# Kernel optimization log

Hardware: AMD Instinct MI355X
Metric: run time of the kernel (lower is better)

Reference implementation:

```python
import jax, jax.numpy as jnp
import numpy as np

RBF_DIM = 64          # args.radius_emb_dim
FOLD_DIM = 128        # args.fold_dim
PROT_RADIUS = 30.0    # args.protein_radius (GaussianSmearing stop)
NP_, NL_, E_ = 100000, 50000, 500000


def gaussian_smearing(d):
    # GaussianSmearing(start=0, stop=PROT_RADIUS, num_gaussians=RBF_DIM)
    offsets = jnp.linspace(0.0, PROT_RADIUS, RBF_DIM, dtype=d.dtype)  # [R]
    coeff = -0.5 / (offsets[1] - offsets[0]) ** 2
    return jnp.exp(coeff * (d[:, None] - offsets[None, :]) ** 2)  # [E, R]


def setup_inputs() -> dict:
    key = jax.random.key(0)
    ks = jax.random.split(key, 12)
    scale = 10.0  # spread positions so distances span [0, PROT_RADIUS]
    pos = lambda k, n: jax.random.normal(k, (n, 3), jnp.float32) * scale
    inp = {
        'lig_pos': pos(ks[0], NL_),
        'prot_pos': pos(ks[1], NP_),
        'prot_pos_Cb': pos(ks[2], NP_),
        'prot_pos_C': pos(ks[3], NP_),
        'prot_pos_O': pos(ks[4], NP_),
        'prot_pos_N': pos(ks[5], NP_),
        'W1': jax.random.normal(ks[6], (5 * RBF_DIM, FOLD_DIM), jnp.float32) * 0.05,
        'b1': jnp.zeros((FOLD_DIM,), jnp.float32),
        'W2': jax.random.normal(ks[7], (FOLD_DIM, FOLD_DIM), jnp.float32) * 0.05,
        'b2': jnp.zeros((FOLD_DIM,), jnp.float32),
        'src': jax.random.randint(ks[8], (E_,), 0, NL_, jnp.int32),   # ligand index per edge
        'dst': jax.random.randint(ks[9], (E_,), 0, NP_, jnp.int32),   # protein index per edge
    }
    return inp


def reference(lig_pos, prot_pos, prot_pos_Cb, prot_pos_C, prot_pos_O, prot_pos_N,
              W1, b1, W2, b2, src, dst):
    lp = lig_pos[src]  # [E, 3] gather of ligand positions
    # 5 distance channels: CA/Cb/C/O/N protein atoms, each RBF-smeared
    feats = [gaussian_smearing(jnp.linalg.norm(lp - p[dst], axis=-1))
             for p in (prot_pos, prot_pos_Cb, prot_pos_C, prot_pos_O, prot_pos_N)]
    edge_attr = jnp.concatenate(feats, axis=-1)  # [E, 5*RBF_DIM]
    h = jax.nn.relu(edge_attr @ W1 + b1)         # [E, FOLD_DIM]
    return h @ W2 + b2                           # [E, FOLD_DIM]
```

## Files before the change

kernel.cpp:

```cpp
#include <hip/hip_runtime.h>
#include <hip/hip_bf16.h>

typedef unsigned short ushort_t;
typedef unsigned int uint_t;
typedef __attribute__((ext_vector_type(8))) short short8;
typedef __attribute__((ext_vector_type(4))) float f32x4;
typedef __attribute__((ext_vector_type(4))) uint_t uint4_t;

#define FOLD 128
#define S_CONST 1.78357580f
#define DS_CONST 0.84932180f

__device__ __forceinline__ ushort_t f2bf(float f) {
    uint_t x = __builtin_bit_cast(uint_t, f);
    x += 0x7FFFu + ((x >> 16) & 1u);
    return (ushort_t)(x >> 16);
}

__device__ __forceinline__ uint_t pack2bf(float flo, float fhi) {
    uint_t xl = __builtin_bit_cast(uint_t, flo);
    uint_t xh = __builtin_bit_cast(uint_t, fhi);
    uint_t rl = (xl + 0x7FFFu + ((xl >> 16) & 1u)) >> 16;
    uint_t rh = (xh + 0x7FFFu + ((xh >> 16) & 1u)) & 0xFFFF0000u;
    return rh | rl;
}

__global__ __launch_bounds__(256) void pack_w(const float* __restrict__ W1,
                                              const float* __restrict__ W2,
                                              ushort_t* __restrict__ W1p,
                                              ushort_t* __restrict__ W2p) {
    int i = blockIdx.x * 256 + threadIdx.x;
    if (i < 40960) {
        int j = i & 7, l = (i >> 3) & 63, nt = (i >> 9) & 7, ks = i >> 12;
        int row = ks * 32 + ((l >> 4) << 3) + j;
        int col = nt * 16 + (l & 15);
        W1p[i] = f2bf(W1[row * FOLD + col]);
    } else if (i < 40960 + 16384) {
        int q = i - 40960;
        int j = q & 7, l = (q >> 3) & 63, nt = (q >> 9) & 7, ks = q >> 12;
        int row = ks * 32 + ((l >> 4) << 3) + j;
        int col = nt * 16 + (l & 15);
        W2p[q] = f2bf(W2[row * FOLD + col]);
    }
}

__global__ __launch_bounds__(256, 2) void fused(
    const float* __restrict__ lig,
    const float* __restrict__ p0, const float* __restrict__ p1,
    const float* __restrict__ p2, const float* __restrict__ p3,
    const float* __restrict__ p4,
    const ushort_t* __restrict__ W1p, const ushort_t* __restrict__ W2p,
    const float* __restrict__ b1, const float* __restrict__ b2,
    const int* __restrict__ src, const int* __restrict__ dst,
    float* __restrict__ out, int E)
{
    __shared__ float d_lds[2][5][32];
    __shared__ alignas(16) uint_t attrU[32 * 160];
    __shared__ ushort_t h_lds[32][136];

    const int t = threadIdx.x;
    const int w = t >> 6;
    const int l = t & 63;
    const int lrow = l & 15, lgrp = l >> 4;
    const int aswz = (lrow & 7) << 2;
    const int ntiles = (E + 31) >> 5;

    const short8* W1v = reinterpret_cast<const short8*>(W1p);
    const short8* W2v = reinterpret_cast<const short8*>(W2p);
    short8 wb1[20], wb2[8];
    #pragma unroll
    for (int ks = 0; ks < 10; ++ks) {
        wb1[2 * ks]     = W1v[(ks * 8 + w * 2 + 0) * 64 + l];
        wb1[2 * ks + 1] = W1v[(ks * 8 + w * 2 + 1) * 64 + l];
    }
    #pragma unroll
    for (int ks = 0; ks < 4; ++ks) {
        wb2[2 * ks]     = W2v[(ks * 8 + w * 2 + 0) * 64 + l];
        wb2[2 * ks + 1] = W2v[(ks * 8 + w * 2 + 1) * 64 + l];
    }
    const float bv0 = b1[w * 32 + lrow];
    const float bv1 = b1[w * 32 + 16 + lrow];
    const float c0  = b2[w * 32 + lrow];
    const float c1  = b2[w * 32 + 16 + lrow];

    const bool gth = (t < 160);
    const int gm = t & 31, gc = t >> 5;
    const float* P = (gc == 0) ? p0 : (gc == 1) ? p1 : (gc == 2) ? p2 : (gc == 3) ? p3 : p4;

    const int m2 = t >> 3, q2 = t & 7;
    const int swz = (m2 & 7) << 2;
    const float ubase = (float)(8 * q2) * DS_CONST;

    int tile = blockIdx.x;
    if (tile >= ntiles) return;

    if (gth) {
        int e = tile * 32 + gm; if (e >= E) e = E - 1;
        int s = src[e], dd = dst[e];
        float dx = lig[3 * s]     - P[3 * dd];
        float dy = lig[3 * s + 1] - P[3 * dd + 1];
        float dz = lig[3 * s + 2] - P[3 * dd + 2];
        d_lds[0][gc][gm] = sqrtf(dx * dx + dy * dy + dz * dz);
    }
    __syncthreads();

    int buf = 0;
    while (true) {
        const int next = tile + gridDim.x;
        const bool havenext = (next < ntiles);

        float ax, ay, az, bx, by, bz;
        if (gth && havenext) {
            int e = next * 32 + gm; if (e >= E) e = E - 1;
            int s = src[e], dd = dst[e];
            ax = lig[3 * s];     bx = P[3 * dd];
            ay = lig[3 * s + 1]; by = P[3 * dd + 1];
            az = lig[3 * s + 2]; bz = P[3 * dd + 2];
        }

        float dv[5];
        #pragma unroll
        for (int c = 0; c < 5; ++c) dv[c] = d_lds[buf][c][m2];
        #pragma unroll
        for (int c = 0; c < 5; ++c) {
            float u0 = __builtin_fmaf(dv[c], S_CONST, -ubase);
            uint4_t vals;
            #pragma unroll
            for (int i = 0; i < 4; ++i) {
                float ua = u0 - (float)(2 * i) * DS_CONST;
                float ub = u0 - (float)(2 * i + 1) * DS_CONST;
                float va = __builtin_amdgcn_exp2f(-(ua * ua));
                float vb = __builtin_amdgcn_exp2f(-(ub * ub));
                vals[i] = pack2bf(va, vb);
            }
            int o = 32 * c + 4 * q2;
            *reinterpret_cast<uint4_t*>(&attrU[m2 * 160 + (o ^ swz)]) = vals;
        }

        if (gth && havenext) {
            float dx = ax - bx, dy = ay - by, dz = az - bz;
            d_lds[buf ^ 1][gc][gm] = sqrtf(dx * dx + dy * dy + dz * dz);
        }
        __syncthreads();

        f32x4 acc00 = {0.f,0.f,0.f,0.f}, acc01 = {0.f,0.f,0.f,0.f};
        f32x4 acc10 = {0.f,0.f,0.f,0.f}, acc11 = {0.f,0.f,0.f,0.f};
        #pragma unroll
        for (int ks = 0; ks < 10; ++ks) {
            int o = ks * 16 + lgrp * 4;
            short8 a0 = *reinterpret_cast<const short8*>(&attrU[lrow * 160 + (o ^ aswz)]);
            short8 a1 = *reinterpret_cast<const short8*>(&attrU[(lrow + 16) * 160 + (o ^ aswz)]);
            acc00 = __builtin_amdgcn_mfma_f32_16x16x32_bf16(a0, wb1[2 * ks],     acc00, 0, 0, 0);
            acc01 = __builtin_amdgcn_mfma_f32_16x16x32_bf16(a0, wb1[2 * ks + 1], acc01, 0, 0, 0);
            acc10 = __builtin_amdgcn_mfma_f32_16x16x32_bf16(a1, wb1[2 * ks],     acc10, 0, 0, 0);
            acc11 = __builtin_amdgcn_mfma_f32_16x16x32_bf16(a1, wb1[2 * ks + 1], acc11, 0, 0, 0);
        }

        #pragma unroll
        for (int j = 0; j < 4; ++j) {
            int r0 = lgrp * 4 + j;
            h_lds[r0][w * 32 + lrow]           = f2bf(fmaxf(acc00[j] + bv0, 0.f));
            h_lds[r0][w * 32 + 16 + lrow]      = f2bf(fmaxf(acc01[j] + bv1, 0.f));
            h_lds[r0 + 16][w * 32 + lrow]      = f2bf(fmaxf(acc10[j] + bv0, 0.f));
            h_lds[r0 + 16][w * 32 + 16 + lrow] = f2bf(fmaxf(acc11[j] + bv1, 0.f));
        }
        __syncthreads();

        f32x4 o00 = {0.f,0.f,0.f,0.f}, o01 = {0.f,0.f,0.f,0.f};
        f32x4 o10 = {0.f,0.f,0.f,0.f}, o11 = {0.f,0.f,0.f,0.f};
        #pragma unroll
        for (int ks = 0; ks < 4; ++ks) {
            short8 a0 = *reinterpret_cast<const short8*>(&h_lds[lrow][ks * 32 + lgrp * 8]);
            short8 a1 = *reinterpret_cast<const short8*>(&h_lds[lrow + 16][ks * 32 + lgrp * 8]);
            o00 = __builtin_amdgcn_mfma_f32_16x16x32_bf16(a0, wb2[2 * ks],     o00, 0, 0, 0);
            o01 = __builtin_amdgcn_mfma_f32_16x16x32_bf16(a0, wb2[2 * ks + 1], o01, 0, 0, 0);
            o10 = __builtin_amdgcn_mfma_f32_16x16x32_bf16(a1, wb2[2 * ks],     o10, 0, 0, 0);
            o11 = __builtin_amdgcn_mfma_f32_16x16x32_bf16(a1, wb2[2 * ks + 1], o11, 0, 0, 0);
        }

        const int e0 = tile * 32;
        #pragma unroll
        for (int j = 0; j < 4; ++j) {
            int r0 = lgrp * 4 + j;
            int eA = e0 + r0;
            int eB = e0 + r0 + 16;
            if (eA < E) {
                out[(size_t)eA * FOLD + w * 32 + lrow]      = o00[j] + c0;
                out[(size_t)eA * FOLD + w * 32 + 16 + lrow] = o01[j] + c1;
            }
            if (eB < E) {
                out[(size_t)eB * FOLD + w * 32 + lrow]      = o10[j] + c0;
                out[(size_t)eB * FOLD + w * 32 + 16 + lrow] = o11[j] + c1;
            }
        }

        if (!havenext) break;
        tile = next;
        buf ^= 1;
    }
}

extern "C" void kernel_launch(void* const* d_in, const int* in_sizes, int n_in,
                              void* d_out, int out_size, void* d_ws, size_t ws_size,
                              hipStream_t stream) {
    const float* lig = (const float*)d_in[0];
    const float* p0  = (const float*)d_in[1];
    const float* p1  = (const float*)d_in[2];
    const float* p2  = (const float*)d_in[3];
    const float* p3  = (const float*)d_in[4];
    const float* p4  = (const float*)d_in[5];
    const float* W1  = (const float*)d_in[6];
    const float* b1  = (const float*)d_in[7];
    const float* W2  = (const float*)d_in[8];
    const float* b2  = (const float*)d_in[9];
    const int* src   = (const int*)d_in[10];
    const int* dst   = (const int*)d_in[11];
    float* out = (float*)d_out;
    const int E = in_sizes[10];

    ushort_t* W1p = (ushort_t*)d_ws;
    ushort_t* W2p = W1p + 40960;

    pack_w<<<(40960 + 16384 + 255) / 256, 256, 0, stream>>>(W1, W2, W1p, W2p);

    int tiles = (E + 31) / 32;
    int nblk = tiles < 1024 ? tiles : 1024;
    fused<<<nblk, 256, 0, stream>>>(lig, p0, p1, p2, p3, p4, W1p, W2p,
                                    b1, b2, src, dst, out, E);
}
```

Measured before the change: 123.7 us.

## Swap MFMA operands to get transposed outputs for vectorized h and output stores

The MFMA operand order is swapped so weights are the A operand and activations the B operand. Each lane then holds four consecutive output columns for one edge. This allows packed bf16 8-byte writes of the hidden layer into a swizzled LDS buffer and 16-byte float4 global stores of the output, replacing scattered 2-byte LDS stores and scalar global stores. Biases become vector loads, and the persistent grid is cut from 1024 to 512 blocks, which lowers the number of resident blocks per CU.

```diff
diff --git a/kernel.cpp b/kernel.cpp
--- a/kernel.cpp
+++ b/kernel.cpp
@@ -6,6 +6,7 @@
 typedef __attribute__((ext_vector_type(8))) short short8;
 typedef __attribute__((ext_vector_type(4))) float f32x4;
 typedef __attribute__((ext_vector_type(4))) uint_t uint4_t;
+typedef __attribute__((ext_vector_type(2))) uint_t uint2_t;
 
 #define FOLD 128
 #define S_CONST 1.78357580f
@@ -17,9 +18,9 @@
     return (ushort_t)(x >> 16);
 }
 
-__device__ __forceinline__ uint_t pack2bf(float flo, float fhi) {
-    uint_t xl = __builtin_bit_cast(uint_t, flo);
-    uint_t xh = __builtin_bit_cast(uint_t, fhi);
+__device__ __forceinline__ uint_t pkbf(float a, float b) {
+    uint_t xl = __builtin_bit_cast(uint_t, a);
+    uint_t xh = __builtin_bit_cast(uint_t, b);
     uint_t rl = (xl + 0x7FFFu + ((xl >> 16) & 1u)) >> 16;
     uint_t rh = (xh + 0x7FFFu + ((xh >> 16) & 1u)) & 0xFFFF0000u;
     return rh | rl;
@@ -56,7 +57,7 @@
 {
     __shared__ float d_lds[2][5][32];
     __shared__ alignas(16) uint_t attrU[32 * 160];
-    __shared__ ushort_t h_lds[32][136];
+    __shared__ alignas(16) uint_t h_u[32 * 64];
 
     const int t = threadIdx.x;
     const int w = t >> 6;
@@ -78,10 +79,11 @@
         wb2[2 * ks]     = W2v[(ks * 8 + w * 2 + 0) * 64 + l];
         wb2[2 * ks + 1] = W2v[(ks * 8 + w * 2 + 1) * 64 + l];
     }
-    const float bv0 = b1[w * 32 + lrow];
-    const float bv1 = b1[w * 32 + 16 + lrow];
-    const float c0  = b2[w * 32 + lrow];
-    const float c1  = b2[w * 32 + 16 + lrow];
+    f32x4 hb1[2], hb2[2];
+    hb1[0] = *reinterpret_cast<const f32x4*>(&b1[w * 32 + lgrp * 4]);
+    hb1[1] = *reinterpret_cast<const f32x4*>(&b1[w * 32 + 16 + lgrp * 4]);
+    hb2[0] = *reinterpret_cast<const f32x4*>(&b2[w * 32 + lgrp * 4]);
+    hb2[1] = *reinterpret_cast<const f32x4*>(&b2[w * 32 + 16 + lgrp * 4]);
 
     const bool gth = (t < 160);
     const int gm = t & 31, gc = t >> 5;
@@ -131,7 +133,7 @@
                 float ub = u0 - (float)(2 * i + 1) * DS_CONST;
                 float va = __builtin_amdgcn_exp2f(-(ua * ua));
                 float vb = __builtin_amdgcn_exp2f(-(ub * ub));
-                vals[i] = pack2bf(va, vb);
+                vals[i] = pkbf(va, vb);
             }
             int o = 32 * c + 4 * q2;
             *reinterpret_cast<uint4_t*>(&attrU[m2 * 160 + (o ^ swz)]) = vals;
@@ -143,54 +145,60 @@
         }
         __syncthreads();
 
-        f32x4 acc00 = {0.f,0.f,0.f,0.f}, acc01 = {0.f,0.f,0.f,0.f};
-        f32x4 acc10 = {0.f,0.f,0.f,0.f}, acc11 = {0.f,0.f,0.f,0.f};
+        f32x4 g1[2][2] = {{{0.f,0.f,0.f,0.f},{0.f,0.f,0.f,0.f}},
+                          {{0.f,0.f,0.f,0.f},{0.f,0.f,0.f,0.f}}};
         #pragma unroll
         for (int ks = 0; ks < 10; ++ks) {
             int o = ks * 16 + lgrp * 4;
-            short8 a0 = *reinterpret_cast<const short8*>(&attrU[lrow * 160 + (o ^ aswz)]);
-            short8 a1 = *reinterpret_cast<const short8*>(&attrU[(lrow + 16) * 160 + (o ^ aswz)]);
-            acc00 = __builtin_amdgcn_mfma_f32_16x16x32_bf16(a0, wb1[2 * ks],     acc00, 0, 0, 0);
-            acc01 = __builtin_amdgcn_mfma_f32_16x16x32_bf16(a0, wb1[2 * ks + 1], acc01, 0, 0, 0);
-            acc10 = __builtin_amdgcn_mfma_f32_16x16x32_bf16(a1, wb1[2 * ks],     acc10, 0, 0, 0);
-            acc11 = __builtin_amdgcn_mfma_f32_16x16x32_bf16(a1, wb1[2 * ks + 1], acc11, 0, 0, 0);
-        }
-
-        #pragma unroll
-        for (int j = 0; j < 4; ++j) {
-            int r0 = lgrp * 4 + j;
-            h_lds[r0][w * 32 + lrow]           = f2bf(fmaxf(acc00[j] + bv0, 0.f));
-            h_lds[r0][w * 32 + 16 + lrow]      = f2bf(fmaxf(acc01[j] + bv1, 0.f));
-            h_lds[r0 + 16][w * 32 + lrow]      = f2bf(fmaxf(acc10[j] + bv0, 0.f));
-            h_lds[r0 + 16][w * 32 + 16 + lrow] = f2bf(fmaxf(acc11[j] + bv1, 0.f));
+            short8 af0 = *reinterpret_cast<const short8*>(&attrU[lrow * 160 + (o ^ aswz)]);
+            short8 af1 = *reinterpret_cast<const short8*>(&attrU[(lrow + 16) * 160 + (o ^ aswz)]);
+            g1[0][0] = __builtin_amdgcn_mfma_f32_16x16x32_bf16(wb1[2 * ks],     af0, g1[0][0], 0, 0, 0);
+            g1[0][1] = __builtin_amdgcn_mfma_f32_16x16x32_bf16(wb1[2 * ks],     af1, g1[0][1], 0, 0, 0);
+            g1[1][0] = __builtin_amdgcn_mfma_f32_16x16x32_bf16(wb1[2 * ks + 1], af0, g1[1][0], 0, 0, 0);
+            g1[1][1] = __builtin_amdgcn_mfma_f32_16x16x32_bf16(wb1[2 * ks + 1], af1, g1[1][1], 0, 0, 0);
+        }
+
+        #pragma unroll
+        for (int nh = 0; nh < 2; ++nh) {
+            #pragma unroll
+            for (int eh = 0; eh < 2; ++eh) {
+                float v0 = fmaxf(g1[nh][eh][0] + hb1[nh][0], 0.f);
+                float v1 = fmaxf(g1[nh][eh][1] + hb1[nh][1], 0.f);
+                float v2 = fmaxf(g1[nh][eh][2] + hb1[nh][2], 0.f);
+                float v3 = fmaxf(g1[nh][eh][3] + hb1[nh][3], 0.f);
+                uint2_t pv;
+                pv[0] = pkbf(v0, v1);
+                pv[1] = pkbf(v2, v3);
+                int e = eh * 16 + lrow;
+                int dw = (w * 16 + nh * 8 + lgrp * 2) ^ ((e & 7) << 2);
+                *reinterpret_cast<uint2_t*>(&h_u[e * 64 + dw]) = pv;
+            }
         }
         __syncthreads();
 
-        f32x4 o00 = {0.f,0.f,0.f,0.f}, o01 = {0.f,0.f,0.f,0.f};
-        f32x4 o10 = {0.f,0.f,0.f,0.f}, o11 = {0.f,0.f,0.f,0.f};
+        f32x4 o2[2][2] = {{{0.f,0.f,0.f,0.f},{0.f,0.f,0.f,0.f}},
+                          {{0.f,0.f,0.f,0.f},{0.f,0.f,0.f,0.f}}};
         #pragma unroll
         for (int ks = 0; ks < 4; ++ks) {
-            short8 a0 = *reinterpret_cast<const short8*>(&h_lds[lrow][ks * 32 + lgrp * 8]);
-            short8 a1 = *reinterpret_cast<const short8*>(&h_lds[lrow + 16][ks * 32 + lgrp * 8]);
-            o00 = __builtin_amdgcn_mfma_f32_16x16x32_bf16(a0, wb2[2 * ks],     o00, 0, 0, 0);
-            o01 = __builtin_amdgcn_mfma_f32_16x16x32_bf16(a0, wb2[2 * ks + 1], o01, 0, 0, 0);
-            o10 = __builtin_amdgcn_mfma_f32_16x16x32_bf16(a1, wb2[2 * ks],     o10, 0, 0, 0);
-            o11 = __builtin_amdgcn_mfma_f32_16x16x32_bf16(a1, wb2[2 * ks + 1], o11, 0, 0, 0);
-        }
-
-        const int e0 = tile * 32;
-        #pragma unroll
-        for (int j = 0; j < 4; ++j) {
-            int r0 = lgrp * 4 + j;
-            int eA = e0 + r0;
-            int eB = e0 + r0 + 16;
-            if (eA < E) {
-                out[(size_t)eA * FOLD + w * 32 + lrow]      = o00[j] + c0;
-                out[(size_t)eA * FOLD + w * 32 + 16 + lrow] = o01[j] + c1;
-            }
-            if (eB < E) {
-                out[(size_t)eB * FOLD + w * 32 + lrow]      = o10[j] + c0;
-                out[(size_t)eB * FOLD + w * 32 + 16 + lrow] = o11[j] + c1;
+            int dw = ks * 16 + lgrp * 4;
+            short8 hf0 = *reinterpret_cast<const short8*>(&h_u[lrow * 64 + (dw ^ aswz)]);
+            short8 hf1 = *reinterpret_cast<const short8*>(&h_u[(lrow + 16) * 64 + (dw ^ aswz)]);
+            o2[0][0] = __builtin_amdgcn_mfma_f32_16x16x32_bf16(wb2[2 * ks],     hf0, o2[0][0], 0, 0, 0);
+            o2[0][1] = __builtin_amdgcn_mfma_f32_16x16x32_bf16(wb2[2 * ks],     hf1, o2[0][1], 0, 0, 0);
+            o2[1][0] = __builtin_amdgcn_mfma_f32_16x16x32_bf16(wb2[2 * ks + 1], hf0, o2[1][0], 0, 0, 0);
+            o2[1][1] = __builtin_amdgcn_mfma_f32_16x16x32_bf16(wb2[2 * ks + 1], hf1, o2[1][1], 0, 0, 0);
+        }
+
+        const int e0i = tile * 32;
+        #pragma unroll
+        for (int nh = 0; nh < 2; ++nh) {
+            #pragma unroll
+            for (int eh = 0; eh < 2; ++eh) {
+                int e = e0i + eh * 16 + lrow;
+                if (e < E) {
+                    f32x4 v = o2[nh][eh] + hb2[nh];
+                    *reinterpret_cast<f32x4*>(&out[(size_t)e * FOLD + w * 32 + nh * 16 + lgrp * 4]) = v;
+                }
             }
         }
 
@@ -224,7 +232,7 @@
     pack_w<<<(40960 + 16384 + 255) / 256, 256, 0, stream>>>(W1, W2, W1p, W2p);
 
     int tiles = (E + 31) / 32;
-    int nblk = tiles < 1024 ? tiles : 1024;
+    int nblk = tiles < 512 ? tiles : 512;
     fused<<<nblk, 256, 0, stream>>>(lig, p0, p1, p2, p3, p4, W1p, W2p,
                                     b1, b2, src, dst, out, E);
 }
```

Result: slower. 129.5 us (+4.7%).
